# Kernel tuning notes

Measured on AMD Instinct MI355X. Metric: run time of the kernel, lower is better.

Reference implementation:

```python
import jax, jax.numpy as jnp
import numpy as np

S, B, H = 1024, 4096, 8  # seq_len, batch, hidden (=input) size


def setup_inputs() -> dict:
    key = jax.random.key(0)
    k0, k1, k2, k3, k4 = jax.random.split(key, 5)
    scale = 1.0 / np.sqrt(H)  # matches torch uniform(-1/sqrt(H), 1/sqrt(H)) magnitude
    return {
        "input_": jax.random.normal(k0, (S, B, H), dtype=jnp.float32),
        "w_ih": jax.random.uniform(k1, (3 * H, H), jnp.float32, -scale, scale),
        "w_hh": jax.random.uniform(k2, (3 * H, H), jnp.float32, -scale, scale),
        "b_ih": jax.random.uniform(k3, (3 * H,), jnp.float32, -scale, scale),
        "b_hh": jax.random.uniform(k4, (3 * H,), jnp.float32, -scale, scale),
    }


def _gru_seq(input_, w_ih, w_hh, b_ih, b_hh):
    # Precompute input-side gate projections for all timesteps in one GEMM:
    # (S, B, 3H); gate order in PyTorch GRU is r, z, n.
    xg = jnp.einsum("sbi,gi->sbg", input_, w_ih) + b_ih
    h0 = jnp.zeros((input_.shape[1], w_hh.shape[1]), dtype=input_.dtype)

    def step(h, xg_t):
        hg = h @ w_hh.T + b_hh                      # (B, 3H)
        xr, xz, xn = jnp.split(xg_t, 3, axis=-1)
        hr, hz, hn = jnp.split(hg, 3, axis=-1)
        r = jax.nn.sigmoid(xr + hr)
        z = jax.nn.sigmoid(xz + hz)
        n = jnp.tanh(xn + r * hn)
        h_new = (1.0 - z) * n + z * h
        return h_new, h_new

    h_last, outputs = jax.lax.scan(step, h0, xg)
    return outputs, h_last[None]  # (S, B, H), (1, B, H) like torch GRU


def reference(input_, w_ih, w_hh, b_ih, b_hh):
    return _gru_seq(input_, w_ih, w_hh, b_ih, b_hh)
```

## Files before the change

### kernel.cpp

```cpp
#include <hip/hip_runtime.h>

#define SS 1024
#define BB 4096
#define HH 8
#define XSTRIDE (BB * HH)

typedef float f32x2 __attribute__((ext_vector_type(2)));

__device__ __forceinline__ float fsig(float x) {
    return __builtin_amdgcn_rcpf(1.0f + __builtin_amdgcn_exp2f(-1.4426950408889634f * x));
}
__device__ __forceinline__ float ftanh(float x) {
    return 1.0f - 2.0f * __builtin_amdgcn_rcpf(1.0f + __builtin_amdgcn_exp2f(2.8853900817779268f * x));
}

__device__ __forceinline__ int dpp_x1(int v) {
    return __builtin_amdgcn_mov_dpp(v, 0xB1, 0xF, 0xF, true);
}
__device__ __forceinline__ int dpp_x2(int v) {
    return __builtin_amdgcn_mov_dpp(v, 0x4E, 0xF, 0xF, true);
}
__device__ __forceinline__ int dpp_x7(int v) {
    return __builtin_amdgcn_mov_dpp(v, 0x141, 0xF, 0xF, true);
}

__device__ __constant__ int MK_[8] = {0, 1, 2, 3, 7, 6, 5, 4};

#define XSTEP(X0, X1, U) do {                                                          \
    f32x2 a0_ = {(X0).x, (X0).y}, a1_ = {(X0).z, (X0).w};                              \
    f32x2 a2_ = {(X1).x, (X1).y}, a3_ = {(X1).z, (X1).w};                              \
    f32x2 sr_ = {bias_r, 0.0f}, sz_ = {bias_z, 0.0f}, sn_ = {bni, 0.0f};               \
    sr_ = __builtin_elementwise_fma(a0_, wri[0], sr_);                                 \
    sr_ = __builtin_elementwise_fma(a1_, wri[1], sr_);                                 \
    sr_ = __builtin_elementwise_fma(a2_, wri[2], sr_);                                 \
    sr_ = __builtin_elementwise_fma(a3_, wri[3], sr_);                                 \
    sz_ = __builtin_elementwise_fma(a0_, wzi[0], sz_);                                 \
    sz_ = __builtin_elementwise_fma(a1_, wzi[1], sz_);                                 \
    sz_ = __builtin_elementwise_fma(a2_, wzi[2], sz_);                                 \
    sz_ = __builtin_elementwise_fma(a3_, wzi[3], sz_);                                 \
    sn_ = __builtin_elementwise_fma(a0_, wni[0], sn_);                                 \
    sn_ = __builtin_elementwise_fma(a1_, wni[1], sn_);                                 \
    sn_ = __builtin_elementwise_fma(a2_, wni[2], sn_);                                 \
    sn_ = __builtin_elementwise_fma(a3_, wni[3], sn_);                                 \
    xr[U] = sr_.x + sr_.y; xz[U] = sz_.x + sz_.y; xn[U] = sn_.x + sn_.y;               \
} while (0)

#define RSTEP(U, SIDX) do {                                                            \
    f32x2 hr2 = {xr[U], 0.0f}, hz2 = {xz[U], 0.0f}, hn2 = {bnh, 0.0f};                 \
    _Pragma("unroll")                                                                  \
    for (int p_ = 0; p_ < 4; ++p_) {                                                   \
        hr2 = __builtin_elementwise_fma(hv2[p_], wrh[p_], hr2);                        \
        hz2 = __builtin_elementwise_fma(hv2[p_], wzh[p_], hz2);                        \
        hn2 = __builtin_elementwise_fma(hv2[p_], wnh[p_], hn2);                        \
    }                                                                                  \
    const float r_ = fsig(hr2.x + hr2.y);                                              \
    const float z_ = fsig(hz2.x + hz2.y);                                              \
    const float n_ = ftanh(xn[U] + r_ * (hn2.x + hn2.y));                              \
    h = n_ + z_ * (h - n_);                                                            \
    const int hb_ = __float_as_int(h);                                                 \
    const int t1_ = dpp_x1(hb_);                                                       \
    const int t2_ = dpp_x2(hb_);                                                       \
    const int t3_ = dpp_x2(t1_);                                                       \
    const int t4_ = dpp_x7(hb_);                                                       \
    const int t5_ = dpp_x7(t1_);                                                       \
    const int t6_ = dpp_x7(t2_);                                                       \
    const int t7_ = dpp_x7(t3_);                                                       \
    hv2[0] = (f32x2){h, __int_as_float(t1_)};                                          \
    hv2[1] = (f32x2){__int_as_float(t2_), __int_as_float(t3_)};                        \
    hv2[2] = (f32x2){__int_as_float(t4_), __int_as_float(t5_)};                        \
    hv2[3] = (f32x2){__int_as_float(t6_), __int_as_float(t7_)};                        \
    op[(size_t)(SIDX) * XSTRIDE] = h;                                                  \
} while (0)

__global__ __launch_bounds__(64, 1) void gru_kernel(
    const float* __restrict__ x,
    const float* __restrict__ w_ih,
    const float* __restrict__ w_hh,
    const float* __restrict__ b_ih,
    const float* __restrict__ b_hh,
    float* __restrict__ out)
{
    const int lane = threadIdx.x;
    const int j = lane & 7;
    const int bg = (blockIdx.x << 3) + (lane >> 3);

    f32x2 wri[4], wzi[4], wni[4];
    #pragma unroll
    for (int p = 0; p < 4; ++p) {
        wri[p] = (f32x2){w_ih[j * 8 + 2 * p],        w_ih[j * 8 + 2 * p + 1]};
        wzi[p] = (f32x2){w_ih[(8 + j) * 8 + 2 * p],  w_ih[(8 + j) * 8 + 2 * p + 1]};
        wni[p] = (f32x2){w_ih[(16 + j) * 8 + 2 * p], w_ih[(16 + j) * 8 + 2 * p + 1]};
    }
    f32x2 wrh[4], wzh[4], wnh[4];
    #pragma unroll
    for (int p = 0; p < 4; ++p) {
        const int c0 = j ^ MK_[2 * p], c1 = j ^ MK_[2 * p + 1];
        wrh[p] = (f32x2){w_hh[j * 8 + c0],        w_hh[j * 8 + c1]};
        wzh[p] = (f32x2){w_hh[(8 + j) * 8 + c0],  w_hh[(8 + j) * 8 + c1]};
        wnh[p] = (f32x2){w_hh[(16 + j) * 8 + c0], w_hh[(16 + j) * 8 + c1]};
    }
    const float bri = b_ih[j], bzi = b_ih[8 + j], bni = b_ih[16 + j];
    const float brh = b_hh[j], bzh = b_hh[8 + j], bnh = b_hh[16 + j];
    const float bias_r = bri + brh, bias_z = bzi + bzh;

    const float* xp = x + (size_t)bg * HH;
    float* op = out + (size_t)bg * HH + j;
    float* hlast = out + (size_t)SS * BB * HH + (size_t)bg * HH + j;

    float4 xA[16], xB[16];

    #pragma unroll
    for (int u = 0; u < 8; ++u) {
        const float* p = xp + (size_t)u * XSTRIDE;
        xA[2 * u]     = *(const float4*)p;
        xA[2 * u + 1] = *(const float4*)(p + 4);
    }
    __builtin_amdgcn_sched_barrier(0);

    float h = 0.0f;
    f32x2 hv2[4] = {{0,0},{0,0},{0,0},{0,0}};
    float xr[8], xz[8], xn[8];

    for (int g = 0; g < 128; g += 2) {
        {
            const float* bp = xp + (size_t)(g + 1) * 8 * XSTRIDE;
            #pragma unroll
            for (int u = 0; u < 8; ++u) {
                const float* p = bp + (size_t)u * XSTRIDE;
                xB[2 * u]     = *(const float4*)p;
                xB[2 * u + 1] = *(const float4*)(p + 4);
            }
        }
        __builtin_amdgcn_sched_barrier(0);
        #pragma unroll
        for (int u = 0; u < 8; ++u) XSTEP(xA[2 * u], xA[2 * u + 1], u);
        #pragma unroll
        for (int u = 0; u < 8; ++u) RSTEP(u, g * 8 + u);
        {
            const int ga = (g + 2 < 128) ? (g + 2) : 127;
            const float* ap = xp + (size_t)ga * 8 * XSTRIDE;
            #pragma unroll
            for (int u = 0; u < 8; ++u) {
                const float* p = ap + (size_t)u * XSTRIDE;
                xA[2 * u]     = *(const float4*)p;
                xA[2 * u + 1] = *(const float4*)(p + 4);
            }
        }
        __builtin_amdgcn_sched_barrier(0);
        #pragma unroll
        for (int u = 0; u < 8; ++u) XSTEP(xB[2 * u], xB[2 * u + 1], u);
        #pragma unroll
        for (int u = 0; u < 8; ++u) RSTEP(u, (g + 1) * 8 + u);
    }
    *hlast = h;
}

extern "C" void kernel_launch(void* const* d_in, const int* in_sizes, int n_in,
                              void* d_out, int out_size, void* d_ws, size_t ws_size,
                              hipStream_t stream) {
    const float* x    = (const float*)d_in[0];
    const float* w_ih = (const float*)d_in[1];
    const float* w_hh = (const float*)d_in[2];
    const float* b_ih = (const float*)d_in[3];
    const float* b_hh = (const float*)d_in[4];
    float* out = (float*)d_out;
    gru_kernel<<<BB / 8, 64, 0, stream>>>(x, w_ih, w_hh, b_ih, b_hh, out);
}
```

Baseline: 151.0 us.

## Interleave two batch chains per thread and prefold activation scales into weights

Each thread now advances two independent GRU recurrences (P and Q batch groups) in lockstep, halving the grid. The aim is instruction-level parallelism to hide the dependent latency of each step. The log2e scale factors for sigmoid and tanh are folded into the weights and biases, removing multiplies from the critical path. Register pressure rises, and the number of resident waves per CU drops.

```diff
diff --git a/kernel.cpp b/kernel.cpp
--- a/kernel.cpp
+++ b/kernel.cpp
@@ -4,15 +4,9 @@
 #define BB 4096
 #define HH 8
 #define XSTRIDE (BB * HH)
+#define NG 256
 
 typedef float f32x2 __attribute__((ext_vector_type(2)));
-
-__device__ __forceinline__ float fsig(float x) {
-    return __builtin_amdgcn_rcpf(1.0f + __builtin_amdgcn_exp2f(-1.4426950408889634f * x));
-}
-__device__ __forceinline__ float ftanh(float x) {
-    return 1.0f - 2.0f * __builtin_amdgcn_rcpf(1.0f + __builtin_amdgcn_exp2f(2.8853900817779268f * x));
-}
 
 __device__ __forceinline__ int dpp_x1(int v) {
     return __builtin_amdgcn_mov_dpp(v, 0xB1, 0xF, 0xF, true);
@@ -26,38 +20,27 @@
 
 __device__ __constant__ int MK_[8] = {0, 1, 2, 3, 7, 6, 5, 4};
 
-#define XSTEP(X0, X1, U) do {                                                          \
+#define XSTEP(C, X0, X1, U) do {                                                       \
     f32x2 a0_ = {(X0).x, (X0).y}, a1_ = {(X0).z, (X0).w};                              \
     f32x2 a2_ = {(X1).x, (X1).y}, a3_ = {(X1).z, (X1).w};                              \
-    f32x2 sr_ = {bias_r, 0.0f}, sz_ = {bias_z, 0.0f}, sn_ = {bni, 0.0f};               \
+    f32x2 sr_ = {bias_r, 0.0f}, sz_ = {bias_z, 0.0f}, sn_ = {bni_s, 0.0f};             \
     sr_ = __builtin_elementwise_fma(a0_, wri[0], sr_);                                 \
+    sz_ = __builtin_elementwise_fma(a0_, wzi[0], sz_);                                 \
+    sn_ = __builtin_elementwise_fma(a0_, wni[0], sn_);                                 \
     sr_ = __builtin_elementwise_fma(a1_, wri[1], sr_);                                 \
+    sz_ = __builtin_elementwise_fma(a1_, wzi[1], sz_);                                 \
+    sn_ = __builtin_elementwise_fma(a1_, wni[1], sn_);                                 \
     sr_ = __builtin_elementwise_fma(a2_, wri[2], sr_);                                 \
+    sz_ = __builtin_elementwise_fma(a2_, wzi[2], sz_);                                 \
+    sn_ = __builtin_elementwise_fma(a2_, wni[2], sn_);                                 \
     sr_ = __builtin_elementwise_fma(a3_, wri[3], sr_);                                 \
-    sz_ = __builtin_elementwise_fma(a0_, wzi[0], sz_);                                 \
-    sz_ = __builtin_elementwise_fma(a1_, wzi[1], sz_);                                 \
-    sz_ = __builtin_elementwise_fma(a2_, wzi[2], sz_);                                 \
     sz_ = __builtin_elementwise_fma(a3_, wzi[3], sz_);                                 \
-    sn_ = __builtin_elementwise_fma(a0_, wni[0], sn_);                                 \
-    sn_ = __builtin_elementwise_fma(a1_, wni[1], sn_);                                 \
-    sn_ = __builtin_elementwise_fma(a2_, wni[2], sn_);                                 \
     sn_ = __builtin_elementwise_fma(a3_, wni[3], sn_);                                 \
-    xr[U] = sr_.x + sr_.y; xz[U] = sz_.x + sz_.y; xn[U] = sn_.x + sn_.y;               \
+    C##xr[U] = sr_.x + sr_.y; C##xz[U] = sz_.x + sz_.y; C##xn[U] = sn_.x + sn_.y;      \
 } while (0)
 
-#define RSTEP(U, SIDX) do {                                                            \
-    f32x2 hr2 = {xr[U], 0.0f}, hz2 = {xz[U], 0.0f}, hn2 = {bnh, 0.0f};                 \
-    _Pragma("unroll")                                                                  \
-    for (int p_ = 0; p_ < 4; ++p_) {                                                   \
-        hr2 = __builtin_elementwise_fma(hv2[p_], wrh[p_], hr2);                        \
-        hz2 = __builtin_elementwise_fma(hv2[p_], wzh[p_], hz2);                        \
-        hn2 = __builtin_elementwise_fma(hv2[p_], wnh[p_], hn2);                        \
-    }                                                                                  \
-    const float r_ = fsig(hr2.x + hr2.y);                                              \
-    const float z_ = fsig(hz2.x + hz2.y);                                              \
-    const float n_ = ftanh(xn[U] + r_ * (hn2.x + hn2.y));                              \
-    h = n_ + z_ * (h - n_);                                                            \
-    const int hb_ = __float_as_int(h);                                                 \
+#define BFLY(C) do {                                                                   \
+    const int hb_ = __float_as_int(C##h);                                              \
     const int t1_ = dpp_x1(hb_);                                                       \
     const int t2_ = dpp_x2(hb_);                                                       \
     const int t3_ = dpp_x2(t1_);                                                       \
@@ -65,11 +48,53 @@
     const int t5_ = dpp_x7(t1_);                                                       \
     const int t6_ = dpp_x7(t2_);                                                       \
     const int t7_ = dpp_x7(t3_);                                                       \
-    hv2[0] = (f32x2){h, __int_as_float(t1_)};                                          \
-    hv2[1] = (f32x2){__int_as_float(t2_), __int_as_float(t3_)};                        \
-    hv2[2] = (f32x2){__int_as_float(t4_), __int_as_float(t5_)};                        \
-    hv2[3] = (f32x2){__int_as_float(t6_), __int_as_float(t7_)};                        \
-    op[(size_t)(SIDX) * XSTRIDE] = h;                                                  \
+    C##hv[0] = (f32x2){C##h, __int_as_float(t1_)};                                     \
+    C##hv[1] = (f32x2){__int_as_float(t2_), __int_as_float(t3_)};                      \
+    C##hv[2] = (f32x2){__int_as_float(t4_), __int_as_float(t5_)};                      \
+    C##hv[3] = (f32x2){__int_as_float(t6_), __int_as_float(t7_)};                      \
+} while (0)
+
+#define RSTEP2(U, SIDX) do {                                                           \
+    f32x2 Pr2 = {Pxr[U], 0.0f}, Qr2 = {Qxr[U], 0.0f};                                  \
+    f32x2 Pz2 = {Pxz[U], 0.0f}, Qz2 = {Qxz[U], 0.0f};                                  \
+    f32x2 Pn2 = {bnh_s, 0.0f},  Qn2 = {bnh_s, 0.0f};                                   \
+    _Pragma("unroll")                                                                  \
+    for (int p_ = 0; p_ < 4; ++p_) {                                                   \
+        Pr2 = __builtin_elementwise_fma(Phv[p_], wrh[p_], Pr2);                        \
+        Qr2 = __builtin_elementwise_fma(Qhv[p_], wrh[p_], Qr2);                        \
+        Pz2 = __builtin_elementwise_fma(Phv[p_], wzh[p_], Pz2);                        \
+        Qz2 = __builtin_elementwise_fma(Qhv[p_], wzh[p_], Qz2);                        \
+        Pn2 = __builtin_elementwise_fma(Phv[p_], wnh[p_], Pn2);                        \
+        Qn2 = __builtin_elementwise_fma(Qhv[p_], wnh[p_], Qn2);                        \
+    }                                                                                  \
+    const float PEr = __builtin_amdgcn_exp2f(Pr2.x + Pr2.y);                           \
+    const float QEr = __builtin_amdgcn_exp2f(Qr2.x + Qr2.y);                           \
+    const float PEz = __builtin_amdgcn_exp2f(Pz2.x + Pz2.y);                           \
+    const float QEz = __builtin_amdgcn_exp2f(Qz2.x + Qz2.y);                           \
+    const float Pr_ = __builtin_amdgcn_rcpf(1.0f + PEr);                               \
+    const float Qr_ = __builtin_amdgcn_rcpf(1.0f + QEr);                               \
+    const float Pz_ = __builtin_amdgcn_rcpf(1.0f + PEz);                               \
+    const float Qz_ = __builtin_amdgcn_rcpf(1.0f + QEz);                               \
+    const float PEn = __builtin_amdgcn_exp2f(fmaf(Pr_, Pn2.x + Pn2.y, Pxn[U]));        \
+    const float QEn = __builtin_amdgcn_exp2f(fmaf(Qr_, Qn2.x + Qn2.y, Qxn[U]));        \
+    const float Pn_ = fmaf(-2.0f, __builtin_amdgcn_rcpf(1.0f + PEn), 1.0f);            \
+    const float Qn_ = fmaf(-2.0f, __builtin_amdgcn_rcpf(1.0f + QEn), 1.0f);            \
+    Ph = Pn_ + Pz_ * (Ph - Pn_);                                                       \
+    Qh = Qn_ + Qz_ * (Qh - Qn_);                                                       \
+    BFLY(P);                                                                           \
+    BFLY(Q);                                                                           \
+    Pop[(size_t)(SIDX) * XSTRIDE] = Ph;                                                \
+    Qop[(size_t)(SIDX) * XSTRIDE] = Qh;                                                \
+} while (0)
+
+#define LOADG(DST, XPTR, GRP) do {                                                     \
+    const float* bp_ = (XPTR) + (size_t)(GRP) * 4 * XSTRIDE;                           \
+    _Pragma("unroll")                                                                  \
+    for (int u_ = 0; u_ < 4; ++u_) {                                                   \
+        const float* p_ = bp_ + (size_t)u_ * XSTRIDE;                                  \
+        DST[2 * u_]     = *(const float4*)p_;                                          \
+        DST[2 * u_ + 1] = *(const float4*)(p_ + 4);                                    \
+    }                                                                                  \
 } while (0)
 
 __global__ __launch_bounds__(64, 1) void gru_kernel(
@@ -82,77 +107,71 @@
 {
     const int lane = threadIdx.x;
     const int j = lane & 7;
-    const int bg = (blockIdx.x << 3) + (lane >> 3);
+    const int bgP = (blockIdx.x << 4) + (lane >> 3);
+    const int bgQ = bgP + 8;
+
+    const float SR = -1.4426950408889634f;
+    const float SN = 2.8853900817779268f;
 
     f32x2 wri[4], wzi[4], wni[4];
     #pragma unroll
     for (int p = 0; p < 4; ++p) {
-        wri[p] = (f32x2){w_ih[j * 8 + 2 * p],        w_ih[j * 8 + 2 * p + 1]};
-        wzi[p] = (f32x2){w_ih[(8 + j) * 8 + 2 * p],  w_ih[(8 + j) * 8 + 2 * p + 1]};
-        wni[p] = (f32x2){w_ih[(16 + j) * 8 + 2 * p], w_ih[(16 + j) * 8 + 2 * p + 1]};
+        wri[p] = (f32x2){SR * w_ih[j * 8 + 2 * p],        SR * w_ih[j * 8 + 2 * p + 1]};
+        wzi[p] = (f32x2){SR * w_ih[(8 + j) * 8 + 2 * p],  SR * w_ih[(8 + j) * 8 + 2 * p + 1]};
+        wni[p] = (f32x2){SN * w_ih[(16 + j) * 8 + 2 * p], SN * w_ih[(16 + j) * 8 + 2 * p + 1]};
     }
     f32x2 wrh[4], wzh[4], wnh[4];
     #pragma unroll
     for (int p = 0; p < 4; ++p) {
         const int c0 = j ^ MK_[2 * p], c1 = j ^ MK_[2 * p + 1];
-        wrh[p] = (f32x2){w_hh[j * 8 + c0],        w_hh[j * 8 + c1]};
-        wzh[p] = (f32x2){w_hh[(8 + j) * 8 + c0],  w_hh[(8 + j) * 8 + c1]};
-        wnh[p] = (f32x2){w_hh[(16 + j) * 8 + c0], w_hh[(16 + j) * 8 + c1]};
+        wrh[p] = (f32x2){SR * w_hh[j * 8 + c0],        SR * w_hh[j * 8 + c1]};
+        wzh[p] = (f32x2){SR * w_hh[(8 + j) * 8 + c0],  SR * w_hh[(8 + j) * 8 + c1]};
+        wnh[p] = (f32x2){SN * w_hh[(16 + j) * 8 + c0], SN * w_hh[(16 + j) * 8 + c1]};
     }
-    const float bri = b_ih[j], bzi = b_ih[8 + j], bni = b_ih[16 + j];
-    const float brh = b_hh[j], bzh = b_hh[8 + j], bnh = b_hh[16 + j];
-    const float bias_r = bri + brh, bias_z = bzi + bzh;
+    const float bias_r = SR * (b_ih[j] + b_hh[j]);
+    const float bias_z = SR * (b_ih[8 + j] + b_hh[8 + j]);
+    const float bni_s  = SN * b_ih[16 + j];
+    const float bnh_s  = SN * b_hh[16 + j];
 
-    const float* xp = x + (size_t)bg * HH;
-    float* op = out + (size_t)bg * HH + j;
-    float* hlast = out + (size_t)SS * BB * HH + (size_t)bg * HH + j;
+    const float* PxP = x + (size_t)bgP * HH;
+    const float* QxP = x + (size_t)bgQ * HH;
+    float* Pop = out + (size_t)bgP * HH + j;
+    float* Qop = out + (size_t)bgQ * HH + j;
+    float* Phl = out + (size_t)SS * BB * HH + (size_t)bgP * HH + j;
+    float* Qhl = out + (size_t)SS * BB * HH + (size_t)bgQ * HH + j;
 
-    float4 xA[16], xB[16];
+    float4 PxA[8], PxB[8], QxA[8], QxB[8];
 
-    #pragma unroll
-    for (int u = 0; u < 8; ++u) {
-        const float* p = xp + (size_t)u * XSTRIDE;
-        xA[2 * u]     = *(const float4*)p;
-        xA[2 * u + 1] = *(const float4*)(p + 4);
-    }
+    LOADG(PxA, PxP, 0);
+    LOADG(QxA, QxP, 0);
     __builtin_amdgcn_sched_barrier(0);
 
-    float h = 0.0f;
-    f32x2 hv2[4] = {{0,0},{0,0},{0,0},{0,0}};
-    float xr[8], xz[8], xn[8];
+    float Ph = 0.0f, Qh = 0.0f;
+    f32x2 Phv[4] = {{0,0},{0,0},{0,0},{0,0}};
+    f32x2 Qhv[4] = {{0,0},{0,0},{0,0},{0,0}};
+    float Pxr[4], Pxz[4], Pxn[4], Qxr[4], Qxz[4], Qxn[4];
 
-    for (int g = 0; g < 128; g += 2) {
+    for (int g = 0; g < NG; g += 2) {
+        LOADG(PxB, PxP, g + 1);
+        LOADG(QxB, QxP, g + 1);
+        __builtin_amdgcn_sched_barrier(0);
+        #pragma unroll
+        for (int u = 0; u < 4; ++u) { XSTEP(P, PxA[2*u], PxA[2*u+1], u); XSTEP(Q, QxA[2*u], QxA[2*u+1], u); }
+        #pragma unroll
+        for (int u = 0; u < 4; ++u) RSTEP2(u, g * 4 + u);
         {
-            const float* bp = xp + (size_t)(g + 1) * 8 * XSTRIDE;
-            #pragma unroll
-            for (int u = 0; u < 8; ++u) {
-                const float* p = bp + (size_t)u * XSTRIDE;
-                xB[2 * u]     = *(const float4*)p;
-                xB[2 * u + 1] = *(const float4*)(p + 4);
-            }
+            const int ga = (g + 2 < NG) ? (g + 2) : (NG - 1);
+            LOADG(PxA, PxP, ga);
+            LOADG(QxA, QxP, ga);
         }
         __builtin_amdgcn_sched_barrier(0);
         #pragma unroll
-        for (int u = 0; u < 8; ++u) XSTEP(xA[2 * u], xA[2 * u + 1], u);
+        for (int u = 0; u < 4; ++u) { XSTEP(P, PxB[2*u], PxB[2*u+1], u); XSTEP(Q, QxB[2*u], QxB[2*u+1], u); }
         #pragma unroll
-        for (int u = 0; u < 8; ++u) RSTEP(u, g * 8 + u);
-        {
-            const int ga = (g + 2 < 128) ? (g + 2) : 127;
-            const float* ap = xp + (size_t)ga * 8 * XSTRIDE;
-            #pragma unroll
-            for (int u = 0; u < 8; ++u) {
-                const float* p = ap + (size_t)u * XSTRIDE;
-                xA[2 * u]     = *(const float4*)p;
-                xA[2 * u + 1] = *(const float4*)(p + 4);
-            }
-        }
-        __builtin_amdgcn_sched_barrier(0);
-        #pragma unroll
-        for (int u = 0; u < 8; ++u) XSTEP(xB[2 * u], xB[2 * u + 1], u);
-        #pragma unroll
-        for (int u = 0; u < 8; ++u) RSTEP(u, (g + 1) * 8 + u);
+        for (int u = 0; u < 4; ++u) RSTEP2(u, (g + 1) * 4 + u);
     }
-    *hlast = h;
+    *Phl = Ph;
+    *Qhl = Qh;
 }
 
 extern "C" void kernel_launch(void* const* d_in, const int* in_sizes, int n_in,
@@ -164,5 +183,5 @@
     const float* b_ih = (const float*)d_in[3];
     const float* b_hh = (const float*)d_in[4];
     float* out = (float*)d_out;
-    gru_kernel<<<BB / 8, 64, 0, stream>>>(x, w_ih, w_hh, b_ih, b_hh, out);
+    gru_kernel<<<BB / 16, 64, 0, stream>>>(x, w_ih, w_hh, b_ih, b_hh, out);
 }
```

New measurement: 273.3 us. 1.81x slower.

## Interleave input projection into recurrence and manage loads with inline asm waitcnt

Applied to the files above, without the earlier changes.

Input loads are now issued with inline-asm global_load_dwordx4 and explicit s_waitcnt vmcnt counts, so two groups are always in flight and only the older group is waited on. The input-gate projections for later timesteps are interleaved with the serial recurrence (between the exp and rcp ops) to hide the dependency-chain latency. The sigmoid/tanh exp-scale constants are folded into the weights and biases, which saves multiplies per step. Output stores become nontemporal. The hand-placed vmcnt counts are fragile: the compiler cannot see the asm loads as producers, so a wrong wait count or a register reuse can read stale data.

```diff
diff --git a/kernel.cpp b/kernel.cpp
--- a/kernel.cpp
+++ b/kernel.cpp
@@ -7,13 +7,6 @@
 
 typedef float f32x2 __attribute__((ext_vector_type(2)));
 
-__device__ __forceinline__ float fsig(float x) {
-    return __builtin_amdgcn_rcpf(1.0f + __builtin_amdgcn_exp2f(-1.4426950408889634f * x));
-}
-__device__ __forceinline__ float ftanh(float x) {
-    return 1.0f - 2.0f * __builtin_amdgcn_rcpf(1.0f + __builtin_amdgcn_exp2f(2.8853900817779268f * x));
-}
-
 __device__ __forceinline__ int dpp_x1(int v) {
     return __builtin_amdgcn_mov_dpp(v, 0xB1, 0xF, 0xF, true);
 }
@@ -26,50 +19,108 @@
 
 __device__ __constant__ int MK_[8] = {0, 1, 2, 3, 7, 6, 5, 4};
 
-#define XSTEP(X0, X1, U) do {                                                          \
-    f32x2 a0_ = {(X0).x, (X0).y}, a1_ = {(X0).z, (X0).w};                              \
-    f32x2 a2_ = {(X1).x, (X1).y}, a3_ = {(X1).z, (X1).w};                              \
-    f32x2 sr_ = {bias_r, 0.0f}, sz_ = {bias_z, 0.0f}, sn_ = {bni, 0.0f};               \
+#define ALOAD(DST, PTR) asm volatile("global_load_dwordx4 %0, %1, off" : "=v"(DST) : "v"(PTR))
+
+#define LOADG(BUF, GRP) do {                                                           \
+    const float* bp_ = xp + (size_t)(GRP) * 8 * XSTRIDE;                               \
+    _Pragma("unroll")                                                                  \
+    for (int u_ = 0; u_ < 8; ++u_) {                                                   \
+        const float* p_ = bp_ + (size_t)u_ * XSTRIDE;                                  \
+        ALOAD(BUF[2 * u_],     p_);                                                    \
+        ALOAD(BUF[2 * u_ + 1], p_ + 4);                                                \
+    }                                                                                  \
+} while (0)
+
+#define WAITV(N) do {                                                                  \
+    asm volatile("s_waitcnt vmcnt(" #N ")" ::: "memory");                              \
+    __builtin_amdgcn_sched_barrier(0);                                                 \
+} while (0)
+
+#define XFULL(BUF, V) do {                                                             \
+    const float4 Xa_ = BUF[2 * (V)], Xb_ = BUF[2 * (V) + 1];                           \
+    f32x2 a0_ = {Xa_.x, Xa_.y}, a1_ = {Xa_.z, Xa_.w};                                  \
+    f32x2 a2_ = {Xb_.x, Xb_.y}, a3_ = {Xb_.z, Xb_.w};                                  \
+    f32x2 sr_ = {bias_r, 0.0f}, sz_ = {bias_z, 0.0f}, sn_ = {bni_s, 0.0f};             \
     sr_ = __builtin_elementwise_fma(a0_, wri[0], sr_);                                 \
+    sz_ = __builtin_elementwise_fma(a0_, wzi[0], sz_);                                 \
+    sn_ = __builtin_elementwise_fma(a0_, wni[0], sn_);                                 \
     sr_ = __builtin_elementwise_fma(a1_, wri[1], sr_);                                 \
+    sz_ = __builtin_elementwise_fma(a1_, wzi[1], sz_);                                 \
+    sn_ = __builtin_elementwise_fma(a1_, wni[1], sn_);                                 \
     sr_ = __builtin_elementwise_fma(a2_, wri[2], sr_);                                 \
+    sz_ = __builtin_elementwise_fma(a2_, wzi[2], sz_);                                 \
+    sn_ = __builtin_elementwise_fma(a2_, wni[2], sn_);                                 \
     sr_ = __builtin_elementwise_fma(a3_, wri[3], sr_);                                 \
-    sz_ = __builtin_elementwise_fma(a0_, wzi[0], sz_);                                 \
-    sz_ = __builtin_elementwise_fma(a1_, wzi[1], sz_);                                 \
-    sz_ = __builtin_elementwise_fma(a2_, wzi[2], sz_);                                 \
     sz_ = __builtin_elementwise_fma(a3_, wzi[3], sz_);                                 \
-    sn_ = __builtin_elementwise_fma(a0_, wni[0], sn_);                                 \
-    sn_ = __builtin_elementwise_fma(a1_, wni[1], sn_);                                 \
-    sn_ = __builtin_elementwise_fma(a2_, wni[2], sn_);                                 \
     sn_ = __builtin_elementwise_fma(a3_, wni[3], sn_);                                 \
-    xr[U] = sr_.x + sr_.y; xz[U] = sz_.x + sz_.y; xn[U] = sn_.x + sn_.y;               \
-} while (0)
-
-#define RSTEP(U, SIDX) do {                                                            \
-    f32x2 hr2 = {xr[U], 0.0f}, hz2 = {xz[U], 0.0f}, hn2 = {bnh, 0.0f};                 \
+    xr[(V)] = sr_.x + sr_.y; xz[(V)] = sz_.x + sz_.y; xn[(V)] = sn_.x + sn_.y;         \
+} while (0)
+
+#define GROUP(BUF, SBASE) do {                                                         \
+    XFULL(BUF, 0);                                                                     \
+    XFULL(BUF, 1);                                                                     \
     _Pragma("unroll")                                                                  \
-    for (int p_ = 0; p_ < 4; ++p_) {                                                   \
-        hr2 = __builtin_elementwise_fma(hv2[p_], wrh[p_], hr2);                        \
-        hz2 = __builtin_elementwise_fma(hv2[p_], wzh[p_], hz2);                        \
-        hn2 = __builtin_elementwise_fma(hv2[p_], wnh[p_], hn2);                        \
+    for (int u = 0; u < 8; ++u) {                                                      \
+        f32x2 hr2 = {xr[u], 0.0f}, hz2 = {xz[u], 0.0f}, hn2 = {bnh_s, 0.0f};           \
+        _Pragma("unroll")                                                              \
+        for (int p_ = 0; p_ < 4; ++p_) {                                               \
+            hr2 = __builtin_elementwise_fma(hv2[p_], wrh[p_], hr2);                    \
+            hz2 = __builtin_elementwise_fma(hv2[p_], wzh[p_], hz2);                    \
+            hn2 = __builtin_elementwise_fma(hv2[p_], wnh[p_], hn2);                    \
+        }                                                                              \
+        const float srr = hr2.x + hr2.y;                                               \
+        const float szz = hz2.x + hz2.y;                                               \
+        const float snn = hn2.x + hn2.y;                                               \
+        const bool W = (u + 2 < 8);                                                    \
+        f32x2 sr_, sz_, sn_;                                                           \
+        if (W) {                   \
+            const float4 Xa_ = BUF[2 * (u + 2)];                                       \
+            f32x2 a0_ = {Xa_.x, Xa_.y}, a1_ = {Xa_.z, Xa_.w};                          \
+            sr_ = (f32x2){bias_r, 0.0f}; sz_ = (f32x2){bias_z, 0.0f};                  \
+            sn_ = (f32x2){bni_s, 0.0f};                                                \
+            sr_ = __builtin_elementwise_fma(a0_, wri[0], sr_);                         \
+            sz_ = __builtin_elementwise_fma(a0_, wzi[0], sz_);                         \
+            sn_ = __builtin_elementwise_fma(a0_, wni[0], sn_);                         \
+            sr_ = __builtin_elementwise_fma(a1_, wri[1], sr_);                         \
+            sz_ = __builtin_elementwise_fma(a1_, wzi[1], sz_);                         \
+            sn_ = __builtin_elementwise_fma(a1_, wni[1], sn_);                         \
+        }                                                                              \
+        const float er = __builtin_amdgcn_exp2f(srr);                                  \
+        const float ez = __builtin_amdgcn_exp2f(szz);                                  \
+        if (W) {                     \
+            const float4 Xb_ = BUF[2 * (u + 2) + 1];                                   \
+            f32x2 a2_ = {Xb_.x, Xb_.y}, a3_ = {Xb_.z, Xb_.w};                          \
+            sr_ = __builtin_elementwise_fma(a2_, wri[2], sr_);                         \
+            sz_ = __builtin_elementwise_fma(a2_, wzi[2], sz_);                         \
+            sn_ = __builtin_elementwise_fma(a2_, wni[2], sn_);                         \
+            sr_ = __builtin_elementwise_fma(a3_, wri[3], sr_);                         \
+            sz_ = __builtin_elementwise_fma(a3_, wzi[3], sz_);                         \
+            sn_ = __builtin_elementwise_fma(a3_, wni[3], sn_);                         \
+        }                                                                              \
+        const float r_ = __builtin_amdgcn_rcpf(1.0f + er);                             \
+        const float z_ = __builtin_amdgcn_rcpf(1.0f + ez);                             \
+        if (W) {                                \
+            xr[u + 2] = sr_.x + sr_.y;                                                 \
+            xz[u + 2] = sz_.x + sz_.y;                                                 \
+            xn[u + 2] = sn_.x + sn_.y;                                                 \
+        }                                                                              \
+        const float en = __builtin_amdgcn_exp2f(fmaf(r_, snn, xn[u]));                 \
+        const float n_ = fmaf(-2.0f, __builtin_amdgcn_rcpf(1.0f + en), 1.0f);          \
+        h = n_ + z_ * (h - n_);                                                        \
+        const int hb_ = __float_as_int(h);                                             \
+        const int t1_ = dpp_x1(hb_);                                                   \
+        const int t2_ = dpp_x2(hb_);                                                   \
+        const int t3_ = dpp_x2(t1_);                                                   \
+        const int t4_ = dpp_x7(hb_);                                                   \
+        const int t5_ = dpp_x7(t1_);                                                   \
+        const int t6_ = dpp_x7(t2_);                                                   \
+        const int t7_ = dpp_x7(t3_);                                                   \
+        hv2[0] = (f32x2){h, __int_as_float(t1_)};                                      \
+        hv2[1] = (f32x2){__int_as_float(t2_), __int_as_float(t3_)};                    \
+        hv2[2] = (f32x2){__int_as_float(t4_), __int_as_float(t5_)};                    \
+        hv2[3] = (f32x2){__int_as_float(t6_), __int_as_float(t7_)};                    \
+        __builtin_nontemporal_store(h, &op[(size_t)((SBASE) + u) * XSTRIDE]);          \
     }                                                                                  \
-    const float r_ = fsig(hr2.x + hr2.y);                                              \
-    const float z_ = fsig(hz2.x + hz2.y);                                              \
-    const float n_ = ftanh(xn[U] + r_ * (hn2.x + hn2.y));                              \
-    h = n_ + z_ * (h - n_);                                                            \
-    const int hb_ = __float_as_int(h);                                                 \
-    const int t1_ = dpp_x1(hb_);                                                       \
-    const int t2_ = dpp_x2(hb_);                                                       \
-    const int t3_ = dpp_x2(t1_);                                                       \
-    const int t4_ = dpp_x7(hb_);                                                       \
-    const int t5_ = dpp_x7(t1_);                                                       \
-    const int t6_ = dpp_x7(t2_);                                                       \
-    const int t7_ = dpp_x7(t3_);                                                       \
-    hv2[0] = (f32x2){h, __int_as_float(t1_)};                                          \
-    hv2[1] = (f32x2){__int_as_float(t2_), __int_as_float(t3_)};                        \
-    hv2[2] = (f32x2){__int_as_float(t4_), __int_as_float(t5_)};                        \
-    hv2[3] = (f32x2){__int_as_float(t6_), __int_as_float(t7_)};                        \
-    op[(size_t)(SIDX) * XSTRIDE] = h;                                                  \
 } while (0)
 
 __global__ __launch_bounds__(64, 1) void gru_kernel(
@@ -84,24 +135,28 @@
     const int j = lane & 7;
     const int bg = (blockIdx.x << 3) + (lane >> 3);
 
+    const float SR = -1.4426950408889634f;
+    const float SN = 2.8853900817779268f;
+
     f32x2 wri[4], wzi[4], wni[4];
     #pragma unroll
     for (int p = 0; p < 4; ++p) {
-        wri[p] = (f32x2){w_ih[j * 8 + 2 * p],        w_ih[j * 8 + 2 * p + 1]};
-        wzi[p] = (f32x2){w_ih[(8 + j) * 8 + 2 * p],  w_ih[(8 + j) * 8 + 2 * p + 1]};
-        wni[p] = (f32x2){w_ih[(16 + j) * 8 + 2 * p], w_ih[(16 + j) * 8 + 2 * p + 1]};
+        wri[p] = (f32x2){SR * w_ih[j * 8 + 2 * p],        SR * w_ih[j * 8 + 2 * p + 1]};
+        wzi[p] = (f32x2){SR * w_ih[(8 + j) * 8 + 2 * p],  SR * w_ih[(8 + j) * 8 + 2 * p + 1]};
+        wni[p] = (f32x2){SN * w_ih[(16 + j) * 8 + 2 * p], SN * w_ih[(16 + j) * 8 + 2 * p + 1]};
     }
     f32x2 wrh[4], wzh[4], wnh[4];
     #pragma unroll
     for (int p = 0; p < 4; ++p) {
         const int c0 = j ^ MK_[2 * p], c1 = j ^ MK_[2 * p + 1];
-        wrh[p] = (f32x2){w_hh[j * 8 + c0],        w_hh[j * 8 + c1]};
-        wzh[p] = (f32x2){w_hh[(8 + j) * 8 + c0],  w_hh[(8 + j) * 8 + c1]};
-        wnh[p] = (f32x2){w_hh[(16 + j) * 8 + c0], w_hh[(16 + j) * 8 + c1]};
+        wrh[p] = (f32x2){SR * w_hh[j * 8 + c0],        SR * w_hh[j * 8 + c1]};
+        wzh[p] = (f32x2){SR * w_hh[(8 + j) * 8 + c0],  SR * w_hh[(8 + j) * 8 + c1]};
+        wnh[p] = (f32x2){SN * w_hh[(16 + j) * 8 + c0], SN * w_hh[(16 + j) * 8 + c1]};
     }
-    const float bri = b_ih[j], bzi = b_ih[8 + j], bni = b_ih[16 + j];
-    const float brh = b_hh[j], bzh = b_hh[8 + j], bnh = b_hh[16 + j];
-    const float bias_r = bri + brh, bias_z = bzi + bzh;
+    const float bias_r = SR * (b_ih[j] + b_hh[j]);
+    const float bias_z = SR * (b_ih[8 + j] + b_hh[8 + j]);
+    const float bni_s  = SN * b_ih[16 + j];
+    const float bnh_s  = SN * b_hh[16 + j];
 
     const float* xp = x + (size_t)bg * HH;
     float* op = out + (size_t)bg * HH + j;
@@ -109,48 +164,27 @@
 
     float4 xA[16], xB[16];
 
-    #pragma unroll
-    for (int u = 0; u < 8; ++u) {
-        const float* p = xp + (size_t)u * XSTRIDE;
-        xA[2 * u]     = *(const float4*)p;
-        xA[2 * u + 1] = *(const float4*)(p + 4);
-    }
-    __builtin_amdgcn_sched_barrier(0);
+    LOADG(xA, 0);
+    LOADG(xB, 1);
+    WAITV(16);
 
     float h = 0.0f;
     f32x2 hv2[4] = {{0,0},{0,0},{0,0},{0,0}};
     float xr[8], xz[8], xn[8];
 
     for (int g = 0; g < 128; g += 2) {
-        {
-            const float* bp = xp + (size_t)(g + 1) * 8 * XSTRIDE;
-            #pragma unroll
-            for (int u = 0; u < 8; ++u) {
-                const float* p = bp + (size_t)u * XSTRIDE;
-                xB[2 * u]     = *(const float4*)p;
-                xB[2 * u + 1] = *(const float4*)(p + 4);
-            }
-        }
-        __builtin_amdgcn_sched_barrier(0);
-        #pragma unroll
-        for (int u = 0; u < 8; ++u) XSTEP(xA[2 * u], xA[2 * u + 1], u);
-        #pragma unroll
-        for (int u = 0; u < 8; ++u) RSTEP(u, g * 8 + u);
+        GROUP(xA, g * 8);
         {
             const int ga = (g + 2 < 128) ? (g + 2) : 127;
-            const float* ap = xp + (size_t)ga * 8 * XSTRIDE;
-            #pragma unroll
-            for (int u = 0; u < 8; ++u) {
-                const float* p = ap + (size_t)u * XSTRIDE;
-                xA[2 * u]     = *(const float4*)p;
-                xA[2 * u + 1] = *(const float4*)(p + 4);
-            }
+            LOADG(xA, ga);
         }
-        __builtin_amdgcn_sched_barrier(0);
-        #pragma unroll
-        for (int u = 0; u < 8; ++u) XSTEP(xB[2 * u], xB[2 * u + 1], u);
-        #pragma unroll
-        for (int u = 0; u < 8; ++u) RSTEP(u, (g + 1) * 8 + u);
+        WAITV(24);
+        GROUP(xB, (g + 1) * 8);
+        {
+            const int gb = (g + 3 < 128) ? (g + 3) : 127;
+            LOADG(xB, gb);
+        }
+        WAITV(24);
     }
     *hlast = h;
 }
```

Measured after the change: 134.8 us. -10.7%, faster.
